# Performance work log

Measured on AMD Instinct MI355X. Metric: run time of the kernel, lower is better.

Reference implementation:

```python
import jax, jax.numpy as jnp
import numpy as np

D = 128      # d_model
H = 8        # n_heads
HD = D // H  # head_dim = 16
E = 256      # n_experts
R = 32       # kv_lora_rank
B, T = 4, 512
EPS = 1e-6


def _dense_init(k, fi, fo):
    s = float(1.0 / np.sqrt(fi))
    return jax.random.uniform(k, (fi, fo), minval=-s, maxval=s, dtype=jnp.float32)


def setup_inputs() -> dict:
    key = jax.random.key(0)
    ks = jax.random.split(key, 16)
    rng = np.random.RandomState(42)
    Q, _ = np.linalg.qr(rng.randn(D, D))
    glim = float(np.sqrt(6.0 / (D + D)))
    return {
        'x': jax.random.normal(ks[0], (B, T, D), dtype=jnp.float32),
        'g1': jnp.ones((D,), jnp.float32),
        'qW': _dense_init(ks[1], D, D), 'qb': jnp.zeros((D,), jnp.float32),
        'kdW': _dense_init(ks[2], D, R), 'kdb': jnp.zeros((R,), jnp.float32),
        'kuW': _dense_init(ks[3], R, 2 * D), 'kub': jnp.zeros((2 * D,), jnp.float32),
        'oW': _dense_init(ks[4], D, D), 'ob': jnp.zeros((D,), jnp.float32),
        'rot': jnp.asarray(Q, jnp.float32),
        'tq_scale': jnp.ones((D,), jnp.float32),
        's1W': _dense_init(ks[5], D, D), 's1b': jnp.zeros((D,), jnp.float32),
        's2W': _dense_init(ks[6], D, D), 's2b': jnp.zeros((D,), jnp.float32),
        'g2': jnp.ones((D,), jnp.float32),
        'gateW': _dense_init(ks[7], D, E), 'gateb': jnp.zeros((E,), jnp.float32),
        'expW': jax.random.uniform(ks[8], (E, D, D), minval=-glim, maxval=glim, dtype=jnp.float32),
        'm1W': _dense_init(ks[9], D, D), 'm1b': jnp.zeros((D,), jnp.float32),
        'm2W': _dense_init(ks[10], D, D), 'm2b': jnp.zeros((D,), jnp.float32),
    }


def _rmsnorm(x, g):
    return g * (x / jnp.sqrt(jnp.mean(x * x, axis=-1, keepdims=True) + EPS))


def _swiglu(x, w1, b1, w2, b2):
    gate = x @ w1 + b1
    return gate * jax.nn.sigmoid(gate) * (x @ w2 + b2)


def _mla(x, qW, qb, kdW, kdb, kuW, kub, oW, ob):
    b, t = x.shape[0], x.shape[1]
    q = (x @ qW + qb).reshape(b, t, H, HD)
    kv = ((x @ kdW + kdb) @ kuW + kub).reshape(b, t, H, 2 * HD)
    k, v = jnp.split(kv, 2, axis=-1)
    q = jax.nn.elu(q) + 1.0
    k = jax.nn.elu(k) + 1.0
    # linear attention: context[b,h,d,e] = sum_t k[b,t,h,d] v[b,t,h,e]
    context = jnp.einsum('bthd,bthe->bhde', k, v)
    out = jnp.einsum('bthd,bhde->bthe', q, context)
    k_sum = jnp.sum(k, axis=1)  # [b,h,d]
    z = 1.0 / (jnp.einsum('bthd,bhd->bth', q, k_sum) + EPS)
    out = out * z[..., None]
    return out.reshape(b, t, D) @ oW + ob


def _turbo_quant(x, rot, scale):
    x = x @ rot
    mag = jnp.sqrt(jnp.mean(x * x, axis=-1, keepdims=True) + EPS)
    phase = x / mag
    qp = jnp.clip(phase * 127.0, -127.0, 127.0) / 127.0
    phase = jax.lax.stop_gradient(qp - phase) + phase  # straight-through
    return phase * mag * scale


def _moe(h, gateW, gateb, expW, m1W, m1b, m2W, m2b):
    gate_scores = jax.nn.softmax(h @ gateW + gateb, axis=-1)  # [B,T,E]
    top_vals, top_idx = jax.lax.top_k(gate_scores, 2)
    top_w = top_vals / (jnp.sum(top_vals, axis=-1, keepdims=True) + EPS)
    # dense all-expert compute as in the original module
    eo = jnp.einsum('btd,edo->bteo', h, expW)  # [B,T,E,D]
    mask = jnp.sum(jax.nn.one_hot(top_idx, E, dtype=h.dtype) * top_w[..., None], axis=2)  # [B,T,E]
    wavg = jnp.einsum('bteo,bte->bto', eo, mask)
    wavg = _swiglu(wavg, m1W, m1b, m2W, m2b)
    diff_sq = jnp.square(eo - wavg[:, :, None, :])
    wvar = jnp.einsum('bteo,bte->bto', diff_sq, mask)
    consensus = jnp.exp(-jnp.mean(wvar, axis=-1))  # [B,T]
    return wavg, consensus


def reference(x, g1, qW, qb, kdW, kdb, kuW, kub, oW, ob, rot, tq_scale,
              s1W, s1b, s2W, s2b, g2, gateW, gateb, expW, m1W, m1b, m2W, m2b):
    attn_out = _turbo_quant(_mla(_rmsnorm(x, g1), qW, qb, kdW, kdb, kuW, kub, oW, ob), rot, tq_scale)
    x = x + _swiglu(attn_out, s1W, s1b, s2W, s2b)
    moe_out, consensus = _moe(_rmsnorm(x, g2), gateW, gateb, expW, m1W, m1b, m2W, m2b)
    return x + moe_out, consensus
```

## Files before the change

### kernel.cpp

```cpp
#include <hip/hip_runtime.h>
#include <math.h>

static constexpr int Dd    = 128;
static constexpr int NH    = 8;
static constexpr int NE    = 256;
static constexpr int RR    = 32;
static constexpr int TT    = 512;
static constexpr int NTOK  = 2048;
static constexpr int SLOTS = 256;
#define EPSF 1e-6f

static constexpr int FK_KV    = 0;
static constexpr int FD_CTX   = 32;
static constexpr int FD_OR    = 36;
static constexpr int FD_RG    = 37;
static constexpr int FD_ROOT  = 45;
static constexpr int FD_EXP   = 46;

__device__ __forceinline__ float elu1(float v) { return v > 0.f ? v + 1.f : expf(v); }
__device__ __forceinline__ float sigm(float v) { return 1.f / (1.f + expf(-v)); }

__device__ __forceinline__ void flag_add(int* p) {
  __hip_atomic_fetch_add(p, 1, __ATOMIC_RELEASE, __HIP_MEMORY_SCOPE_AGENT);
}
__device__ __forceinline__ void flag_wait(int* p, int tgt) {
  int c = 0;
  while (__hip_atomic_load(p, __ATOMIC_ACQUIRE, __HIP_MEMORY_SCOPE_AGENT) < tgt) {
    __builtin_amdgcn_s_sleep(2);
    if (++c > (1 << 27)) break;
  }
}

struct AParams {
  const float *x, *g1, *qW, *qb, *kdW, *kdb, *kuW, *kub, *oW, *ob, *rot, *tqs;
  const float *s1W, *s1b, *s2W, *s2b, *g2, *gateW, *gateb, *expW;
  const float *m1W, *m1b, *m2W, *m2b;
  float *kvbuf, *ctx, *ksum, *oR, *bR, *h2buf, *ybuf, *out;
  int *cnt, *slottok, *flags;
};

__global__ __launch_bounds__(512, 4) void k_all(AParams P) {
  const int tid = threadIdx.x;
  const int bid = blockIdx.x;
  const int t  = tid >> 7;
  const int j2 = tid & 127;
  const int lane = tid & 63;
  const int n0 = bid * 4;
  const int b = bid >> 7;

  __shared__ float sh[64 * 32];
  __shared__ float4 bufA[128];
  __shared__ float4 bufB[128];
  __shared__ float ws1[8], ws2[8];
  __shared__ float4 rtmp[2];
  __shared__ float wvS[4][4]; __shared__ int wiS[4][4];
  __shared__ float zS[4][4];
  __shared__ int sE[4][2]; __shared__ int sSlot[4][2]; __shared__ float sWt[4][2];
  __shared__ __align__(16) float hT[128 * 20];
  __shared__ float4 y1T[128], y2T[128], inT[128], sT[128];

  float4* kpart4 = (float4*)hT;
  float4* kdT4   = (float4*)(hT + 1024);

  const float xv_s = P.x[(n0 + t) * Dd + j2];
  {
    float v = xv_s * xv_s;
#pragma unroll
    for (int o = 32; o > 0; o >>= 1) v += __shfl_xor(v, o, 64);
    if (lane == 0) ws1[tid >> 6] = v;
  }
  __syncthreads();
  {
    float ss = ws1[2 * t] + ws1[2 * t + 1];
    ((float*)&bufB[j2])[t] = P.g1[j2] * xv_s * rsqrtf(ss * (1.f / 128.f) + EPSF);
  }
  __syncthreads();

  {
    float acc = 0.f;
    const float* Wp = P.qW + j2;
#pragma unroll 8
    for (int i = 0; i < 128; i++) acc += ((const float*)&bufB[i])[t] * Wp[i * Dd];
    ((float*)&bufA[j2])[t] = elu1(acc + P.qb[j2]);
  }

  if (tid < 256) {
    int col = tid & 31, ksp = tid >> 5;
    float a0 = 0, a1 = 0, a2 = 0, a3 = 0;
    const float* Wp = P.kdW + (ksp * 16) * RR + col;
#pragma unroll
    for (int i = 0; i < 16; i++) {
      float4 h4 = bufB[ksp * 16 + i];
      float w = Wp[i * RR];
      a0 += h4.x * w; a1 += h4.y * w; a2 += h4.z * w; a3 += h4.w * w;
    }
    kpart4[ksp * 32 + col] = make_float4(a0, a1, a2, a3);
  }
  __syncthreads();
  if (tid < 32) {
    float bb = P.kdb[tid];
    float s0 = bb, s1 = bb, s2 = bb, s3 = bb;
#pragma unroll
    for (int k = 0; k < 8; k++) {
      float4 p = kpart4[k * 32 + tid];
      s0 += p.x; s1 += p.y; s2 += p.z; s3 += p.w;
    }
    kdT4[tid] = make_float4(s0, s1, s2, s3);
  }
  __syncthreads();

  if (tid < 256) {
    const int col = tid;
    float a0 = 0, a1 = 0, a2 = 0, a3 = 0;
    const float* Wp = P.kuW + col;
#pragma unroll
    for (int r = 0; r < 32; r++) {
      float4 k4 = kdT4[r];
      float w = Wp[r * 256];
      a0 += k4.x * w; a1 += k4.y * w; a2 += k4.z * w; a3 += k4.w * w;
    }
    float bb = P.kub[col];
    bool isk = (col & 31) < 16;
    float v0 = a0 + bb, v1 = a1 + bb, v2 = a2 + bb, v3 = a3 + bb;
    P.kvbuf[(n0 + 0) * 256 + col] = isk ? elu1(v0) : v0;
    P.kvbuf[(n0 + 1) * 256 + col] = isk ? elu1(v1) : v1;
    P.kvbuf[(n0 + 2) * 256 + col] = isk ? elu1(v2) : v2;
    P.kvbuf[(n0 + 3) * 256 + col] = isk ? elu1(v3) : v3;
  }
  __threadfence();
  __syncthreads();
  if (tid == 0) flag_add(&P.flags[FK_KV + b * 8 + ((bid & 127) >> 4)]);

  if (bid < 256) {
    const int bh = bid >> 3, c = bid & 7;
    const int bb = bh >> 3, h = bh & 7;
    if (tid == 0) flag_wait(&P.flags[FK_KV + bb * 8 + c], 16);
    __syncthreads();
    __threadfence();
#pragma unroll
    for (int r = 0; r < 4; r++) {
      int lin = r * 512 + tid;
      int tok = lin >> 5, off = lin & 31;
      sh[lin] = P.kvbuf[((bb * TT + c * 64 + tok) * 256) + h * 32 + off];
    }
    __syncthreads();
    if (tid < 256) {
      const int d = tid >> 4, e = tid & 15;
      float acc = 0.f, ks = 0.f;
#pragma unroll 4
      for (int tk = 0; tk < 64; tk++) {
        float kk = sh[tk * 32 + d];
        acc += kk * sh[tk * 32 + 16 + e];
        ks += kk;
      }
      atomicAdd(&P.ctx[bh * 256 + d * 16 + e], acc);
      if (e == 0) atomicAdd(&P.ksum[bh * 16 + d], ks);
    }
    __threadfence();
    __syncthreads();
    if (tid == 0) flag_add(&P.flags[FD_CTX + bb]);
  } else if (bid < 288) {
    int idx = (bid - 256) * 512 + tid;
    int row = idx >> 7, col = idx & 127;
    const float* ow = P.oW + row * 128;
    float acc = 0.f;
#pragma unroll 8
    for (int k = 0; k < 128; k++) acc += ow[k] * P.rot[k * 128 + col];
    P.oR[idx] = acc;
    __threadfence();
    __syncthreads();
    if (tid == 0) flag_add(&P.flags[FD_OR]);
  } else if (bid == 288) {
    if (tid < 128) {
      float acc = 0.f;
#pragma unroll 8
      for (int k = 0; k < 128; k++) acc += P.ob[k] * P.rot[k * 128 + tid];
      P.bR[tid] = acc;
    }
    __threadfence();
    __syncthreads();
    if (tid == 0) flag_add(&P.flags[FD_OR]);
  }

  if (tid == 0) flag_wait(&P.flags[FD_CTX + b], 64);
  if (tid == 1) flag_wait(&P.flags[FD_OR], 33);
  __syncthreads();
  __threadfence();

  if (tid < 128) {
    int h = j2 >> 4, e = j2 & 15;
    const float* cpt = P.ctx + (b * NH + h) * 256;
    const float* kpt = P.ksum + (b * NH + h) * 16;
    float num[4] = {0, 0, 0, 0}, den[4] = {0, 0, 0, 0};
#pragma unroll
    for (int d = 0; d < 16; d++) {
      float cx = cpt[d * 16 + e], ks = kpt[d];
      float4 q4 = bufA[h * 16 + d];
      num[0] += q4.x * cx; num[1] += q4.y * cx; num[2] += q4.z * cx; num[3] += q4.w * cx;
      den[0] += q4.x * ks; den[1] += q4.y * ks; den[2] += q4.z * ks; den[3] += q4.w * ks;
    }
#pragma unroll
    for (int tt = 0; tt < 4; tt++) ((float*)&bufB[j2])[tt] = num[tt] / (den[tt] + EPSF);
  }
  __syncthreads();

  {
    float acc = 0.f;
    const float* Wp = P.oR + j2;
#pragma unroll 8
    for (int i = 0; i < 128; i++) acc += ((const float*)&bufB[i])[t] * Wp[i * Dd];
    float tot = acc + P.bR[j2];
    float v = tot * tot;
#pragma unroll
    for (int o = 32; o > 0; o >>= 1) v += __shfl_xor(v, o, 64);
    if (lane == 0) ws1[tid >> 6] = v;
    __syncthreads();
    float ss = ws1[2 * t] + ws1[2 * t + 1];
    float mag = sqrtf(ss * (1.f / 128.f) + EPSF);
    float zc = fminf(fmaxf(tot, -mag), mag);
    ((float*)&bufA[j2])[t] = zc * P.tqs[j2];
  }
  __syncthreads();

  float xn_s;
  {
    float a1 = 0.f, a2 = 0.f;
    const float* W1 = P.s1W + j2;
    const float* W2 = P.s2W + j2;
#pragma unroll 8
    for (int i = 0; i < 128; i++) {
      float h = ((const float*)&bufA[i])[t];
      a1 += h * W1[i * Dd];
      a2 += h * W2[i * Dd];
    }
    float gv = a1 + P.s1b[j2], uv = a2 + P.s2b[j2];
    xn_s = xv_s + gv * sigm(gv) * uv;
    float v = xn_s * xn_s;
#pragma unroll
    for (int o = 32; o > 0; o >>= 1) v += __shfl_xor(v, o, 64);
    if (lane == 0) ws2[tid >> 6] = v;
    ((float*)&bufB[j2])[t] = P.g2[j2] * xn_s;
  }
  __syncthreads();

  float val[4]; float r2v[4];
  {
#pragma unroll
    for (int tt = 0; tt < 4; tt++)
      r2v[tt] = rsqrtf((ws2[2 * tt] + ws2[2 * tt + 1]) * (1.f / 128.f) + EPSF);
    if (tid < 256) {
      const int col = tid;
      float a[4] = {0, 0, 0, 0};
      const float* Wp = P.gateW + col;
#pragma unroll 4
      for (int i = 0; i < 128; i++) {
        float4 h4 = bufB[i];
        float w = Wp[i * NE];
        a[0] += h4.x * w; a[1] += h4.y * w; a[2] += h4.z * w; a[3] += h4.w * w;
      }
      float bb = P.gateb[col];
#pragma unroll
      for (int tt = 0; tt < 4; tt++) val[tt] = a[tt] * r2v[tt] + bb;
    }
    P.h2buf[(n0 + t) * Dd + j2] = P.g2[j2] * xn_s * r2v[t];
  }
  __syncthreads();

  float m1[4]; int i1[4];
  {
    if (tid < 256) {
      float bv[4]; int bi[4];
#pragma unroll
      for (int tt = 0; tt < 4; tt++) { bv[tt] = val[tt]; bi[tt] = tid; }
#pragma unroll
      for (int o = 32; o > 0; o >>= 1) {
#pragma unroll
        for (int tt = 0; tt < 4; tt++) {
          float wv = __shfl_xor(bv[tt], o, 64);
          int wi = __shfl_xor(bi[tt], o, 64);
          if (wv > bv[tt] || (wv == bv[tt] && wi < bi[tt])) { bv[tt] = wv; bi[tt] = wi; }
        }
      }
      if (lane == 0) {
#pragma unroll
        for (int tt = 0; tt < 4; tt++) { wvS[tid >> 6][tt] = bv[tt]; wiS[tid >> 6][tt] = bi[tt]; }
      }
    }
    __syncthreads();
    if (tid < 256) {
#pragma unroll
      for (int tt = 0; tt < 4; tt++) {
        m1[tt] = wvS[0][tt]; i1[tt] = wiS[0][tt];
#pragma unroll
        for (int w = 1; w < 4; w++) {
          float cv = wvS[w][tt]; int ci = wiS[w][tt];
          if (cv > m1[tt] || (cv == m1[tt] && ci < i1[tt])) { m1[tt] = cv; i1[tt] = ci; }
        }
      }
    }
    __syncthreads();
  }
  float m2[4]; int i2[4];
  {
    if (tid < 256) {
      float bv[4]; int bi[4];
#pragma unroll
      for (int tt = 0; tt < 4; tt++) {
        bv[tt] = (tid == i1[tt]) ? -INFINITY : val[tt];
        bi[tt] = tid;
      }
#pragma unroll
      for (int o = 32; o > 0; o >>= 1) {
#pragma unroll
        for (int tt = 0; tt < 4; tt++) {
          float wv = __shfl_xor(bv[tt], o, 64);
          int wi = __shfl_xor(bi[tt], o, 64);
          if (wv > bv[tt] || (wv == bv[tt] && wi < bi[tt])) { bv[tt] = wv; bi[tt] = wi; }
        }
      }
      if (lane == 0) {
#pragma unroll
        for (int tt = 0; tt < 4; tt++) { wvS[tid >> 6][tt] = bv[tt]; wiS[tid >> 6][tt] = bi[tt]; }
      }
    }
    __syncthreads();
    if (tid < 256) {
#pragma unroll
      for (int tt = 0; tt < 4; tt++) {
        m2[tt] = wvS[0][tt]; i2[tt] = wiS[0][tt];
#pragma unroll
        for (int w = 1; w < 4; w++) {
          float cv = wvS[w][tt]; int ci = wiS[w][tt];
          if (cv > m2[tt] || (cv == m2[tt] && ci < i2[tt])) { m2[tt] = cv; i2[tt] = ci; }
        }
      }
    }
    __syncthreads();
  }
  {
    if (tid < 256) {
      float v[4];
#pragma unroll
      for (int tt = 0; tt < 4; tt++) v[tt] = expf(val[tt] - m1[tt]);
#pragma unroll
      for (int o = 32; o > 0; o >>= 1) {
#pragma unroll
        for (int tt = 0; tt < 4; tt++) v[tt] += __shfl_xor(v[tt], o, 64);
      }
      if (lane == 0) {
#pragma unroll
        for (int tt = 0; tt < 4; tt++) zS[tid >> 6][tt] = v[tt];
      }
    }
    __syncthreads();
  }
  if (tid < 4) {
    int tt = tid, tok = n0 + tt;
    float Z = zS[0][tt] + zS[1][tt] + zS[2][tt] + zS[3][tt];
    float p1 = 1.f / Z;
    float p2 = expf(m2[tt] - m1[tt]) / Z;
    float s = p1 + p2 + EPSF;
    int e1 = i1[tt], e2 = i2[tt];
    int s1 = atomicAdd(&P.cnt[e1], 1); if (s1 > SLOTS - 1) s1 = SLOTS - 1;
    int s2 = atomicAdd(&P.cnt[e2], 1); if (s2 > SLOTS - 1) s2 = SLOTS - 1;
    int sl1 = e1 * SLOTS + s1, sl2 = e2 * SLOTS + s2;
    P.slottok[sl1] = tok; P.slottok[sl2] = tok;
    sE[tt][0] = e1; sE[tt][1] = e2;
    sSlot[tt][0] = sl1; sSlot[tt][1] = sl2;
    sWt[tt][0] = p1 / s; sWt[tt][1] = p2 / s;
  }

  __threadfence();
  __syncthreads();
  if (tid == 0) {
    int grp = bid >> 6;
    int prev = __hip_atomic_fetch_add(&P.flags[FD_RG + grp], 1,
                                      __ATOMIC_ACQ_REL, __HIP_MEMORY_SCOPE_AGENT);
    if (prev == 63) flag_add(&P.flags[FD_ROOT]);
    flag_wait(&P.flags[FD_ROOT], 8);
  }
  __syncthreads();
  __threadfence();

  {
    const int e = bid >> 1, sub = bid & 1;
    int n = __hip_atomic_load(&P.cnt[e], __ATOMIC_RELAXED, __HIP_MEMORY_SCOPE_AGENT);
    if (n > SLOTS) n = SLOTS;
    const int base = e * SLOTS;
    const float* Wp = P.expW + (size_t)e * Dd * Dd + j2;
    for (int t0 = sub * 16; t0 < n; t0 += 32) {
      int m = n - t0; if (m > 16) m = 16;
      __syncthreads();
      for (int tt = t; tt < m; tt += 4) {
        int tok = P.slottok[base + t0 + tt];
        hT[j2 * 20 + tt] = P.h2buf[tok * Dd + j2];
      }
      __syncthreads();
      float acc[4] = {0, 0, 0, 0};
#pragma unroll 8
      for (int i = 0; i < 128; i++) {
        float w = Wp[i * Dd];
        float4 h4 = *(const float4*)&hT[i * 20 + t * 4];
        acc[0] += h4.x * w; acc[1] += h4.y * w; acc[2] += h4.z * w; acc[3] += h4.w * w;
      }
#pragma unroll
      for (int k = 0; k < 4; k++) {
        int tt = t * 4 + k;
        if (tt < m) P.ybuf[(size_t)(base + t0 + tt) * Dd + j2] = acc[k];
      }
    }
    __threadfence();
    __syncthreads();
    if (tid == 0) flag_add(&P.flags[FD_EXP + e]);
  }

  if (tid < 8) {
    int tt = tid >> 1, sl = tid & 1;
    flag_wait(&P.flags[FD_EXP + sE[tt][sl]], 2);
  }
  __syncthreads();
  __threadfence();

  {
    float y1 = P.ybuf[(size_t)sSlot[t][0] * Dd + j2];
    float y2 = P.ybuf[(size_t)sSlot[t][1] * Dd + j2];
    ((float*)&y1T[j2])[t] = y1;
    ((float*)&y2T[j2])[t] = y2;
    ((float*)&inT[j2])[t] = sWt[t][0] * y1 + sWt[t][1] * y2;
  }
  __syncthreads();

  {
    float a1 = 0.f, a2 = 0.f;
    const float* W1 = P.m1W + j2;
    const float* W2 = P.m2W + j2;
#pragma unroll 8
    for (int i = 0; i < 128; i++) {
      float h = ((const float*)&inT[i])[t];
      a1 += h * W1[i * Dd];
      a2 += h * W2[i * Dd];
    }
    float gv = a1 + P.m1b[j2], uv = a2 + P.m2b[j2];
    float sv = gv * sigm(gv) * uv;
    ((float*)&sT[j2])[t] = sv;
    P.out[(n0 + t) * Dd + j2] = xn_s + sv;
  }
  __syncthreads();

  if (tid < 128) {
    float v[4];
#pragma unroll
    for (int tt = 0; tt < 4; tt++) {
      float sv = ((const float*)&sT[j2])[tt];
      float d1 = ((const float*)&y1T[j2])[tt] - sv;
      float d2 = ((const float*)&y2T[j2])[tt] - sv;
      v[tt] = sWt[tt][0] * d1 * d1 + sWt[tt][1] * d2 * d2;
    }
#pragma unroll
    for (int o = 32; o > 0; o >>= 1) {
#pragma unroll
      for (int tt = 0; tt < 4; tt++) v[tt] += __shfl_xor(v[tt], o, 64);
    }
    if (lane == 0) rtmp[tid >> 6] = make_float4(v[0], v[1], v[2], v[3]);
  }
  __syncthreads();
  if (tid < 4) {
    float s = ((const float*)&rtmp[0])[tid] + ((const float*)&rtmp[1])[tid];
    P.out[NTOK * Dd + n0 + tid] = expf(-s * (1.f / 128.f));
  }
}

__global__ __launch_bounds__(512) void k_pre_fb(
    const float* __restrict__ x, const float* __restrict__ g1,
    const float* __restrict__ qW, const float* __restrict__ qb,
    const float* __restrict__ kdW, const float* __restrict__ kdb,
    const float* __restrict__ kuW, const float* __restrict__ kub,
    const float* __restrict__ oW, const float* __restrict__ ob,
    const float* __restrict__ rot,
    float* __restrict__ qbuf, float* __restrict__ kvbuf,
    float* __restrict__ ctx, float* __restrict__ ksum,
    int* __restrict__ cnt,
    float* __restrict__ oR, float* __restrict__ bR) {
  const int tid = threadIdx.x;
  const int bid = blockIdx.x;
  const int j = tid & 127, g = tid >> 7;
  const int lane = tid & 63;
  const int n0 = bid * 4;

  __shared__ float4 h1T[128];
  __shared__ float4 part[3][128];
  __shared__ float4 kpart[8][32];
  __shared__ float4 kdT[32];
  __shared__ float4 kupart[256];
  __shared__ float4 rtmp[2];

  if (bid == 0) {
    for (int i = tid; i < 32 * 256; i += 512) ctx[i] = 0.f;
    ksum[tid] = 0.f;
    if (tid < NE) cnt[tid] = 0;
  }

  float xv[4];
  if (tid < 128) {
    float v[4];
#pragma unroll
    for (int t = 0; t < 4; t++) { xv[t] = x[(n0 + t) * Dd + j]; v[t] = xv[t] * xv[t]; }
#pragma unroll
    for (int o = 32; o > 0; o >>= 1) {
#pragma unroll
      for (int t = 0; t < 4; t++) v[t] += __shfl_xor(v[t], o, 64);
    }
    if (lane == 0) rtmp[tid >> 6] = make_float4(v[0], v[1], v[2], v[3]);
  }
  __syncthreads();
  if (tid < 128) {
    float g1j = g1[j];
#pragma unroll
    for (int t = 0; t < 4; t++) {
      float ss = ((const float*)&rtmp[0])[t] + ((const float*)&rtmp[1])[t];
      ((float*)&h1T[j])[t] = g1j * xv[t] * rsqrtf(ss * (1.f / 128.f) + EPSF);
    }
  }
  __syncthreads();

  {
    float a0 = 0, a1 = 0, a2 = 0, a3 = 0;
    const float* Wp = qW + (g * 32) * Dd + j;
#pragma unroll 16
    for (int i = 0; i < 32; i++) {
      float4 h4 = h1T[g * 32 + i];
      float w = Wp[i * Dd];
      a0 += h4.x * w; a1 += h4.y * w; a2 += h4.z * w; a3 += h4.w * w;
    }
    if (g) part[g - 1][j] = make_float4(a0, a1, a2, a3);
    __syncthreads();
    if (g == 0) {
      float4 p0 = part[0][j], p1 = part[1][j], p2 = part[2][j];
      float bb = qb[j];
      qbuf[(n0 + 0) * Dd + j] = elu1(a0 + p0.x + p1.x + p2.x + bb);
      qbuf[(n0 + 1) * Dd + j] = elu1(a1 + p0.y + p1.y + p2.y + bb);
      qbuf[(n0 + 2) * Dd + j] = elu1(a2 + p0.z + p1.z + p2.z + bb);
      qbuf[(n0 + 3) * Dd + j] = elu1(a3 + p0.w + p1.w + p2.w + bb);
    }
    __syncthreads();
  }

  if (tid < 256) {
    int col = tid & 31, ksp = tid >> 5;
    float a0 = 0, a1 = 0, a2 = 0, a3 = 0;
    const float* Wp = kdW + (ksp * 16) * RR + col;
// ... 453 lines not shown
#pragma unroll
    for (int t = 0; t < 4; t++) {
      float sv = ((const float*)&sT[j])[t];
      float d1 = ((const float*)&y1T[j])[t] - sv;
      float d2 = ((const float*)&y2T[j])[t] - sv;
      v[t] = sWt[t][0] * d1 * d1 + sWt[t][1] * d2 * d2;
    }
#pragma unroll
    for (int o = 32; o > 0; o >>= 1) {
#pragma unroll
      for (int t = 0; t < 4; t++) v[t] += __shfl_xor(v[t], o, 64);
    }
    if (lane == 0) rtmp[tid >> 6] = make_float4(v[0], v[1], v[2], v[3]);
  }
  __syncthreads();
  if (tid < 4) {
    float s = ((const float*)&rtmp[0])[tid] + ((const float*)&rtmp[1])[tid];
    out[NTOK * Dd + n0 + tid] = expf(-s * (1.f / 128.f));
  }
}

extern "C" void kernel_launch(void* const* d_in, const int* in_sizes, int n_in,
                              void* d_out, int out_size, void* d_ws, size_t ws_size,
                              hipStream_t stream) {
  const float* x   = (const float*)d_in[0];
  const float* g1  = (const float*)d_in[1];
  const float* qW  = (const float*)d_in[2];
  const float* qb  = (const float*)d_in[3];
  const float* kdW = (const float*)d_in[4];
  const float* kdb = (const float*)d_in[5];
  const float* kuW = (const float*)d_in[6];
  const float* kub = (const float*)d_in[7];
  const float* oW  = (const float*)d_in[8];
  const float* ob  = (const float*)d_in[9];
  const float* rot = (const float*)d_in[10];
  const float* tqs = (const float*)d_in[11];
  const float* s1W = (const float*)d_in[12];
  const float* s1b = (const float*)d_in[13];
  const float* s2W = (const float*)d_in[14];
  const float* s2b = (const float*)d_in[15];
  const float* g2  = (const float*)d_in[16];
  const float* gW  = (const float*)d_in[17];
  const float* gb  = (const float*)d_in[18];
  const float* eW  = (const float*)d_in[19];
  const float* m1W = (const float*)d_in[20];
  const float* m1b = (const float*)d_in[21];
  const float* m2W = (const float*)d_in[22];
  const float* m2b = (const float*)d_in[23];
  float* out = (float*)d_out;
  float* ws  = (float*)d_ws;

  float* ctx     = ws;
  float* ksum    = ws + 8192;
  int*   cnt     = (int*)(ws + 8704);
  int*   flags   = (int*)(ws + 8960);
  float* oR      = ws + 9472;
  float* bR      = ws + 25856;
  float* kvbuf   = ws + 25984;
  float* h2buf   = ws + 550272;
  float* ybuf    = ws + 812416;
  int*   slottok = (int*)(ws + 9201024);
  float* qbuf    = ws + 9266560;
  float* xnbuf   = ws + 9528704;
  float* gw      = ws + 9790848;
  int*   tokslot = (int*)(ws + 9794944);

  hipMemsetAsync(ws, 0, (8192 + 512 + 256 + 512) * sizeof(float), stream);

  AParams p;
  p.x = x; p.g1 = g1; p.qW = qW; p.qb = qb; p.kdW = kdW; p.kdb = kdb;
  p.kuW = kuW; p.kub = kub; p.oW = oW; p.ob = ob; p.rot = rot; p.tqs = tqs;
  p.s1W = s1W; p.s1b = s1b; p.s2W = s2W; p.s2b = s2b; p.g2 = g2;
  p.gateW = gW; p.gateb = gb; p.expW = eW;
  p.m1W = m1W; p.m1b = m1b; p.m2W = m2W; p.m2b = m2b;
  p.kvbuf = kvbuf; p.ctx = ctx; p.ksum = ksum; p.oR = oR; p.bR = bR;
  p.h2buf = h2buf; p.ybuf = ybuf; p.out = out;
  p.cnt = cnt; p.slottok = slottok; p.flags = flags;

  void* args[] = {(void*)&p};
  hipError_t err = hipErrorUnknown;
  int nb = 0;
  if (hipOccupancyMaxActiveBlocksPerMultiprocessor(
          &nb, reinterpret_cast<const void*>(&k_all), 512, 0) == hipSuccess &&
      nb >= 2) {
    err = hipLaunchCooperativeKernel((void*)k_all, dim3(NTOK / 4), dim3(512),
                                     args, 0u, stream);
  }
  if (err == hipSuccess) return;

  k_pre_fb<<<NTOK / 4, 512, 0, stream>>>(x, g1, qW, qb, kdW, kdb, kuW, kub,
                                         oW, ob, rot, qbuf, kvbuf, ctx, ksum,
                                         cnt, oR, bR);
  k_ctx_fb<<<256, 256, 0, stream>>>(kvbuf, ctx, ksum);
  k_mid_fb<<<NTOK / 4, 512, 0, stream>>>(x, qbuf, ctx, ksum, oR, bR, tqs,
                                         s1W, s1b, s2W, s2b, g2, gW, gb,
                                         xnbuf, h2buf, gw, tokslot, slottok, cnt);
  k_exp_fb<<<NE * 2, 512, 0, stream>>>(h2buf, slottok, cnt, eW, ybuf);
  k_post_fb<<<NTOK / 4, 512, 0, stream>>>(xnbuf, ybuf, tokslot, gw,
                                          m1W, m1b, m2W, m2b, out);
}
```

Before: 164.5 us.

## Process sixteen tokens per block in fused cooperative kernel, shrinking grid to 128

The persistent cooperative kernel now handles 16 tokens per block instead of 4, so each weight load feeds four tokens per thread in every projection. The grid drops from 512 to 128 blocks, and the context and expert phases loop over several tasks per block. The two-level grid barrier becomes a single counter. Fewer blocks means less barrier and flag overhead and more weight reuse, at the cost of using only 128 of the GPU's compute units, more serial work per block, and higher register pressure.

```diff
diff --git a/kernel.cpp b/kernel.cpp
--- a/kernel.cpp
+++ b/kernel.cpp
@@ -8,12 +8,13 @@
 static constexpr int TT    = 512;
 static constexpr int NTOK  = 2048;
 static constexpr int SLOTS = 256;
+static constexpr int TPB   = 16;
+static constexpr int GRID  = NTOK / TPB;
 #define EPSF 1e-6f
 
 static constexpr int FK_KV    = 0;
 static constexpr int FD_CTX   = 32;
 static constexpr int FD_OR    = 36;
-static constexpr int FD_RG    = 37;
 static constexpr int FD_ROOT  = 45;
 static constexpr int FD_EXP   = 46;
 
@@ -39,147 +40,152 @@
   int *cnt, *slottok, *flags;
 };
 
-__global__ __launch_bounds__(512, 4) void k_all(AParams P) {
+__global__ __launch_bounds__(512) void k_all(AParams P) {
   const int tid = threadIdx.x;
   const int bid = blockIdx.x;
-  const int t  = tid >> 7;
+  const int tg = tid >> 7;
   const int j2 = tid & 127;
   const int lane = tid & 63;
-  const int n0 = bid * 4;
-  const int b = bid >> 7;
-
-  __shared__ float sh[64 * 32];
-  __shared__ float4 bufA[128];
-  __shared__ float4 bufB[128];
-  __shared__ float ws1[8], ws2[8];
-  __shared__ float4 rtmp[2];
+  const int wv = tid >> 6;
+  const int n0 = bid * TPB;
+  const int b = bid >> 5;
+
+  __shared__ float bufA[128][16];
+  __shared__ float bufB[128][16];
+  __shared__ float kdT[RR][16];
+  __shared__ float wsA[8][4], wsB[8][4];
+  __shared__ float r2S[16];
   __shared__ float wvS[4][4]; __shared__ int wiS[4][4];
   __shared__ float zS[4][4];
-  __shared__ int sE[4][2]; __shared__ int sSlot[4][2]; __shared__ float sWt[4][2];
-  __shared__ __align__(16) float hT[128 * 20];
-  __shared__ float4 y1T[128], y2T[128], inT[128], sT[128];
-
-  float4* kpart4 = (float4*)hT;
-  float4* kdT4   = (float4*)(hT + 1024);
-
-  const float xv_s = P.x[(n0 + t) * Dd + j2];
-  {
-    float v = xv_s * xv_s;
-#pragma unroll
-    for (int o = 32; o > 0; o >>= 1) v += __shfl_xor(v, o, 64);
-    if (lane == 0) ws1[tid >> 6] = v;
-  }
-  __syncthreads();
-  {
-    float ss = ws1[2 * t] + ws1[2 * t + 1];
-    ((float*)&bufB[j2])[t] = P.g1[j2] * xv_s * rsqrtf(ss * (1.f / 128.f) + EPSF);
-  }
-  __syncthreads();
-
-  {
+  __shared__ int sE[16][2]; __shared__ int sSlot[16][2]; __shared__ float sWt[16][2];
+  __shared__ __align__(16) float arena[2560];
+
+  float xv_r[4];
+  {
+    float v[4];
+#pragma unroll
+    for (int r = 0; r < 4; r++) {
+      xv_r[r] = P.x[(n0 + tg * 4 + r) * Dd + j2];
+      v[r] = xv_r[r] * xv_r[r];
+    }
+#pragma unroll
+    for (int o = 32; o > 0; o >>= 1)
+#pragma unroll
+      for (int r = 0; r < 4; r++) v[r] += __shfl_xor(v[r], o, 64);
+    if (lane == 0) {
+      wsA[wv][0] = v[0]; wsA[wv][1] = v[1]; wsA[wv][2] = v[2]; wsA[wv][3] = v[3];
+    }
+  }
+  __syncthreads();
+  {
+    float g1j = P.g1[j2];
+#pragma unroll
+    for (int r = 0; r < 4; r++) {
+      float ss = wsA[2 * tg][r] + wsA[2 * tg + 1][r];
+      bufB[j2][tg * 4 + r] = g1j * xv_r[r] * rsqrtf(ss * (1.f / 128.f) + EPSF);
+    }
+  }
+  __syncthreads();
+
+  {
+    float acc[4] = {0, 0, 0, 0};
+    const float* Wp = P.qW + j2;
+#pragma unroll 4
+    for (int i = 0; i < 128; i++) {
+      float w = Wp[i * Dd];
+#pragma unroll
+      for (int r = 0; r < 4; r++) acc[r] += bufB[i][tg * 4 + r] * w;
+    }
+    float bb = P.qb[j2];
+#pragma unroll
+    for (int r = 0; r < 4; r++) bufA[j2][tg * 4 + r] = elu1(acc[r] + bb);
+  }
+
+  {
+    int col = tid & 31, tok = tid >> 5;
     float acc = 0.f;
-    const float* Wp = P.qW + j2;
-#pragma unroll 8
-    for (int i = 0; i < 128; i++) acc += ((const float*)&bufB[i])[t] * Wp[i * Dd];
-    ((float*)&bufA[j2])[t] = elu1(acc + P.qb[j2]);
-  }
-
-  if (tid < 256) {
-    int col = tid & 31, ksp = tid >> 5;
-    float a0 = 0, a1 = 0, a2 = 0, a3 = 0;
-    const float* Wp = P.kdW + (ksp * 16) * RR + col;
-#pragma unroll
-    for (int i = 0; i < 16; i++) {
-      float4 h4 = bufB[ksp * 16 + i];
-      float w = Wp[i * RR];
-      a0 += h4.x * w; a1 += h4.y * w; a2 += h4.z * w; a3 += h4.w * w;
-    }
-    kpart4[ksp * 32 + col] = make_float4(a0, a1, a2, a3);
-  }
-  __syncthreads();
-  if (tid < 32) {
-    float bb = P.kdb[tid];
-    float s0 = bb, s1 = bb, s2 = bb, s3 = bb;
-#pragma unroll
-    for (int k = 0; k < 8; k++) {
-      float4 p = kpart4[k * 32 + tid];
-      s0 += p.x; s1 += p.y; s2 += p.z; s3 += p.w;
-    }
-    kdT4[tid] = make_float4(s0, s1, s2, s3);
-  }
-  __syncthreads();
-
-  if (tid < 256) {
-    const int col = tid;
-    float a0 = 0, a1 = 0, a2 = 0, a3 = 0;
+    const float* Wp = P.kdW + col;
+#pragma unroll 4
+    for (int i = 0; i < 128; i++) acc += bufB[i][tok] * Wp[i * RR];
+    kdT[col][tok] = acc + P.kdb[col];
+  }
+  __syncthreads();
+
+  {
+    int col = tid & 255, half = tid >> 8;
+    float acc[8] = {0, 0, 0, 0, 0, 0, 0, 0};
     const float* Wp = P.kuW + col;
 #pragma unroll
     for (int r = 0; r < 32; r++) {
-      float4 k4 = kdT4[r];
       float w = Wp[r * 256];
-      a0 += k4.x * w; a1 += k4.y * w; a2 += k4.z * w; a3 += k4.w * w;
+#pragma unroll
+      for (int m = 0; m < 8; m++) acc[m] += kdT[r][half * 8 + m] * w;
     }
     float bb = P.kub[col];
     bool isk = (col & 31) < 16;
-    float v0 = a0 + bb, v1 = a1 + bb, v2 = a2 + bb, v3 = a3 + bb;
-    P.kvbuf[(n0 + 0) * 256 + col] = isk ? elu1(v0) : v0;
-    P.kvbuf[(n0 + 1) * 256 + col] = isk ? elu1(v1) : v1;
-    P.kvbuf[(n0 + 2) * 256 + col] = isk ? elu1(v2) : v2;
-    P.kvbuf[(n0 + 3) * 256 + col] = isk ? elu1(v3) : v3;
+#pragma unroll
+    for (int m = 0; m < 8; m++) {
+      float v = acc[m] + bb;
+      P.kvbuf[(n0 + half * 8 + m) * 256 + col] = isk ? elu1(v) : v;
+    }
   }
   __threadfence();
   __syncthreads();
-  if (tid == 0) flag_add(&P.flags[FK_KV + b * 8 + ((bid & 127) >> 4)]);
-
-  if (bid < 256) {
-    const int bh = bid >> 3, c = bid & 7;
-    const int bb = bh >> 3, h = bh & 7;
-    if (tid == 0) flag_wait(&P.flags[FK_KV + bb * 8 + c], 16);
-    __syncthreads();
-    __threadfence();
-#pragma unroll
-    for (int r = 0; r < 4; r++) {
-      int lin = r * 512 + tid;
-      int tok = lin >> 5, off = lin & 31;
-      sh[lin] = P.kvbuf[((bb * TT + c * 64 + tok) * 256) + h * 32 + off];
-    }
-    __syncthreads();
-    if (tid < 256) {
-      const int d = tid >> 4, e = tid & 15;
-      float acc = 0.f, ks = 0.f;
-#pragma unroll 4
-      for (int tk = 0; tk < 64; tk++) {
-        float kk = sh[tk * 32 + d];
-        acc += kk * sh[tk * 32 + 16 + e];
-        ks += kk;
-      }
-      atomicAdd(&P.ctx[bh * 256 + d * 16 + e], acc);
-      if (e == 0) atomicAdd(&P.ksum[bh * 16 + d], ks);
-    }
-    __threadfence();
-    __syncthreads();
-    if (tid == 0) flag_add(&P.flags[FD_CTX + bb]);
-  } else if (bid < 288) {
-    int idx = (bid - 256) * 512 + tid;
+  if (tid == 0) flag_add(&P.flags[FK_KV + b * 8 + ((bid >> 2) & 7)]);
+
+  if (bid < 32) {
+    int idx = bid * 512 + tid;
     int row = idx >> 7, col = idx & 127;
     const float* ow = P.oW + row * 128;
     float acc = 0.f;
 #pragma unroll 8
     for (int k = 0; k < 128; k++) acc += ow[k] * P.rot[k * 128 + col];
     P.oR[idx] = acc;
-    __threadfence();
-    __syncthreads();
+    __threadfence(); __syncthreads();
     if (tid == 0) flag_add(&P.flags[FD_OR]);
-  } else if (bid == 288) {
+  } else if (bid == 32) {
     if (tid < 128) {
       float acc = 0.f;
 #pragma unroll 8
       for (int k = 0; k < 128; k++) acc += P.ob[k] * P.rot[k * 128 + tid];
       P.bR[tid] = acc;
     }
-    __threadfence();
-    __syncthreads();
+    __threadfence(); __syncthreads();
     if (tid == 0) flag_add(&P.flags[FD_OR]);
+  }
+
+  {
+    float* sh = arena;
+    for (int k = 0; k < 2; k++) {
+      int task = bid + k * 128;
+      int bh = task >> 3, c = task & 7;
+      int bb2 = bh >> 3, h = bh & 7;
+      if (tid == 0) flag_wait(&P.flags[FK_KV + bb2 * 8 + c], 4);
+      __syncthreads();
+      __threadfence();
+#pragma unroll
+      for (int r = 0; r < 4; r++) {
+        int lin = r * 512 + tid;
+        int tok = lin >> 5, off = lin & 31;
+        sh[lin] = P.kvbuf[((bb2 * TT + c * 64 + tok) * 256) + h * 32 + off];
+      }
+      __syncthreads();
+      if (tid < 256) {
+        int d = tid >> 4, e = tid & 15;
+        float acc = 0.f, ks = 0.f;
+#pragma unroll 4
+        for (int tk = 0; tk < 64; tk++) {
+          float kk = sh[tk * 32 + d];
+          acc += kk * sh[tk * 32 + 16 + e];
+          ks += kk;
+        }
+        atomicAdd(&P.ctx[bh * 256 + d * 16 + e], acc);
+        if (e == 0) atomicAdd(&P.ksum[bh * 16 + d], ks);
+      }
+      __threadfence();
+      __syncthreads();
+      if (tid == 0) flag_add(&P.flags[FD_CTX + bb2]);
+    }
   }
 
   if (tid == 0) flag_wait(&P.flags[FD_CTX + b], 64);
@@ -187,7 +193,7 @@
   __syncthreads();
   __threadfence();
 
-  if (tid < 128) {
+  {
     int h = j2 >> 4, e = j2 & 15;
     const float* cpt = P.ctx + (b * NH + h) * 256;
     const float* kpt = P.ksum + (b * NH + h) * 16;
@@ -195,277 +201,332 @@
 #pragma unroll
     for (int d = 0; d < 16; d++) {
       float cx = cpt[d * 16 + e], ks = kpt[d];
-      float4 q4 = bufA[h * 16 + d];
-      num[0] += q4.x * cx; num[1] += q4.y * cx; num[2] += q4.z * cx; num[3] += q4.w * cx;
-      den[0] += q4.x * ks; den[1] += q4.y * ks; den[2] += q4.z * ks; den[3] += q4.w * ks;
-    }
-#pragma unroll
-    for (int tt = 0; tt < 4; tt++) ((float*)&bufB[j2])[tt] = num[tt] / (den[tt] + EPSF);
-  }
-  __syncthreads();
-
-  {
-    float acc = 0.f;
+#pragma unroll
+      for (int r = 0; r < 4; r++) {
+        float qv = bufA[h * 16 + d][tg * 4 + r];
+        num[r] += qv * cx; den[r] += qv * ks;
+      }
+    }
+#pragma unroll
+    for (int r = 0; r < 4; r++) bufB[j2][tg * 4 + r] = num[r] / (den[r] + EPSF);
+  }
+  __syncthreads();
+
+  {
+    float acc[4] = {0, 0, 0, 0};
     const float* Wp = P.oR + j2;
-#pragma unroll 8
-    for (int i = 0; i < 128; i++) acc += ((const float*)&bufB[i])[t] * Wp[i * Dd];
-    float tot = acc + P.bR[j2];
-    float v = tot * tot;
-#pragma unroll
-    for (int o = 32; o > 0; o >>= 1) v += __shfl_xor(v, o, 64);
-    if (lane == 0) ws1[tid >> 6] = v;
-    __syncthreads();
-    float ss = ws1[2 * t] + ws1[2 * t + 1];
-    float mag = sqrtf(ss * (1.f / 128.f) + EPSF);
-    float zc = fminf(fmaxf(tot, -mag), mag);
-    ((float*)&bufA[j2])[t] = zc * P.tqs[j2];
-  }
-  __syncthreads();
-
-  float xn_s;
-  {
-    float a1 = 0.f, a2 = 0.f;
+#pragma unroll 4
+    for (int i = 0; i < 128; i++) {
+      float w = Wp[i * Dd];
+#pragma unroll
+      for (int r = 0; r < 4; r++) acc[r] += bufB[i][tg * 4 + r] * w;
+    }
+    float bRj = P.bR[j2];
+    float tot[4], v[4];
+#pragma unroll
+    for (int r = 0; r < 4; r++) { tot[r] = acc[r] + bRj; v[r] = tot[r] * tot[r]; }
+#pragma unroll
+    for (int o = 32; o > 0; o >>= 1)
+#pragma unroll
+      for (int r = 0; r < 4; r++) v[r] += __shfl_xor(v[r], o, 64);
+    if (lane == 0) {
+      wsA[wv][0] = v[0]; wsA[wv][1] = v[1]; wsA[wv][2] = v[2]; wsA[wv][3] = v[3];
+    }
+    __syncthreads();
+    float scj = P.tqs[j2];
+#pragma unroll
+    for (int r = 0; r < 4; r++) {
+      float ss = wsA[2 * tg][r] + wsA[2 * tg + 1][r];
+      float mag = sqrtf(ss * (1.f / 128.f) + EPSF);
+      float zc = fminf(fmaxf(tot[r], -mag), mag);
+      bufA[j2][tg * 4 + r] = zc * scj;
+    }
+  }
+  __syncthreads();
+
+  float xn_r[4];
+  {
+    float a1[4] = {0, 0, 0, 0}, a2[4] = {0, 0, 0, 0};
     const float* W1 = P.s1W + j2;
     const float* W2 = P.s2W + j2;
+#pragma unroll 4
+    for (int i = 0; i < 128; i++) {
+      float w1 = W1[i * Dd], w2 = W2[i * Dd];
+#pragma unroll
+      for (int r = 0; r < 4; r++) {
+        float h = bufA[i][tg * 4 + r];
+        a1[r] += h * w1; a2[r] += h * w2;
+      }
+    }
+    float b1 = P.s1b[j2], b2 = P.s2b[j2], g2j = P.g2[j2];
+    float v[4];
+#pragma unroll
+    for (int r = 0; r < 4; r++) {
+      float gv = a1[r] + b1, uv = a2[r] + b2;
+      xn_r[r] = xv_r[r] + gv * sigm(gv) * uv;
+      v[r] = xn_r[r] * xn_r[r];
+      bufB[j2][tg * 4 + r] = g2j * xn_r[r];
+    }
+#pragma unroll
+    for (int o = 32; o > 0; o >>= 1)
+#pragma unroll
+      for (int r = 0; r < 4; r++) v[r] += __shfl_xor(v[r], o, 64);
+    if (lane == 0) {
+      wsB[wv][0] = v[0]; wsB[wv][1] = v[1]; wsB[wv][2] = v[2]; wsB[wv][3] = v[3];
+    }
+  }
+  __syncthreads();
+  if (tid < 16) {
+    int tgo = tid >> 2, r = tid & 3;
+    r2S[tid] = rsqrtf((wsB[2 * tgo][r] + wsB[2 * tgo + 1][r]) * (1.f / 128.f) + EPSF);
+  }
+  __syncthreads();
+  {
+#pragma unroll
+    for (int r = 0; r < 4; r++)
+      P.h2buf[(n0 + tg * 4 + r) * Dd + j2] = bufB[j2][tg * 4 + r] * r2S[tg * 4 + r];
+  }
+
+  {
+    float4* gpart = (float4*)arena;
+    for (int grp = 0; grp < 4; grp++) {
+      float val[4]; float r2v[4];
+#pragma unroll
+      for (int t = 0; t < 4; t++) r2v[t] = r2S[grp * 4 + t];
+      {
+        int col = tid & 255, kh = tid >> 8;
+        float a0 = 0, a1 = 0, a2 = 0, a3 = 0;
+        const float* Wp = P.gateW + (kh * 64) * NE + col;
 #pragma unroll 8
-    for (int i = 0; i < 128; i++) {
-      float h = ((const float*)&bufA[i])[t];
-      a1 += h * W1[i * Dd];
-      a2 += h * W2[i * Dd];
-    }
-    float gv = a1 + P.s1b[j2], uv = a2 + P.s2b[j2];
-    xn_s = xv_s + gv * sigm(gv) * uv;
-    float v = xn_s * xn_s;
-#pragma unroll
-    for (int o = 32; o > 0; o >>= 1) v += __shfl_xor(v, o, 64);
-    if (lane == 0) ws2[tid >> 6] = v;
-    ((float*)&bufB[j2])[t] = P.g2[j2] * xn_s;
-  }
-  __syncthreads();
-
-  float val[4]; float r2v[4];
-  {
-#pragma unroll
-    for (int tt = 0; tt < 4; tt++)
-      r2v[tt] = rsqrtf((ws2[2 * tt] + ws2[2 * tt + 1]) * (1.f / 128.f) + EPSF);
-    if (tid < 256) {
-      const int col = tid;
-      float a[4] = {0, 0, 0, 0};
-      const float* Wp = P.gateW + col;
-#pragma unroll 4
-      for (int i = 0; i < 128; i++) {
-        float4 h4 = bufB[i];
-        float w = Wp[i * NE];
-        a[0] += h4.x * w; a[1] += h4.y * w; a[2] += h4.z * w; a[3] += h4.w * w;
-      }
-      float bb = P.gateb[col];
-#pragma unroll
-      for (int tt = 0; tt < 4; tt++) val[tt] = a[tt] * r2v[tt] + bb;
-    }
-    P.h2buf[(n0 + t) * Dd + j2] = P.g2[j2] * xn_s * r2v[t];
-  }
-  __syncthreads();
-
-  float m1[4]; int i1[4];
-  {
-    if (tid < 256) {
-      float bv[4]; int bi[4];
-#pragma unroll
-      for (int tt = 0; tt < 4; tt++) { bv[tt] = val[tt]; bi[tt] = tid; }
-#pragma unroll
-      for (int o = 32; o > 0; o >>= 1) {
-#pragma unroll
-        for (int tt = 0; tt < 4; tt++) {
-          float wv = __shfl_xor(bv[tt], o, 64);
-          int wi = __shfl_xor(bi[tt], o, 64);
-          if (wv > bv[tt] || (wv == bv[tt] && wi < bi[tt])) { bv[tt] = wv; bi[tt] = wi; }
-        }
-      }
-      if (lane == 0) {
-#pragma unroll
-        for (int tt = 0; tt < 4; tt++) { wvS[tid >> 6][tt] = bv[tt]; wiS[tid >> 6][tt] = bi[tt]; }
-      }
-    }
-    __syncthreads();
-    if (tid < 256) {
-#pragma unroll
-      for (int tt = 0; tt < 4; tt++) {
-        m1[tt] = wvS[0][tt]; i1[tt] = wiS[0][tt];
-#pragma unroll
-        for (int w = 1; w < 4; w++) {
-          float cv = wvS[w][tt]; int ci = wiS[w][tt];
-          if (cv > m1[tt] || (cv == m1[tt] && ci < i1[tt])) { m1[tt] = cv; i1[tt] = ci; }
-        }
-      }
-    }
-    __syncthreads();
-  }
-  float m2[4]; int i2[4];
-  {
-    if (tid < 256) {
-      float bv[4]; int bi[4];
-#pragma unroll
-      for (int tt = 0; tt < 4; tt++) {
-        bv[tt] = (tid == i1[tt]) ? -INFINITY : val[tt];
-        bi[tt] = tid;
-      }
-#pragma unroll
-      for (int o = 32; o > 0; o >>= 1) {
-#pragma unroll
-        for (int tt = 0; tt < 4; tt++) {
-          float wv = __shfl_xor(bv[tt], o, 64);
-          int wi = __shfl_xor(bi[tt], o, 64);
-          if (wv > bv[tt] || (wv == bv[tt] && wi < bi[tt])) { bv[tt] = wv; bi[tt] = wi; }
-        }
-      }
-      if (lane == 0) {
-#pragma unroll
-        for (int tt = 0; tt < 4; tt++) { wvS[tid >> 6][tt] = bv[tt]; wiS[tid >> 6][tt] = bi[tt]; }
-      }
-    }
-    __syncthreads();
-    if (tid < 256) {
-#pragma unroll
-      for (int tt = 0; tt < 4; tt++) {
-        m2[tt] = wvS[0][tt]; i2[tt] = wiS[0][tt];
-#pragma unroll
-        for (int w = 1; w < 4; w++) {
-          float cv = wvS[w][tt]; int ci = wiS[w][tt];
-          if (cv > m2[tt] || (cv == m2[tt] && ci < i2[tt])) { m2[tt] = cv; i2[tt] = ci; }
-        }
-      }
-    }
-    __syncthreads();
-  }
-  {
-    if (tid < 256) {
-      float v[4];
-#pragma unroll
-      for (int tt = 0; tt < 4; tt++) v[tt] = expf(val[tt] - m1[tt]);
-#pragma unroll
-      for (int o = 32; o > 0; o >>= 1) {
-#pragma unroll
-        for (int tt = 0; tt < 4; tt++) v[tt] += __shfl_xor(v[tt], o, 64);
-      }
-      if (lane == 0) {
-#pragma unroll
-        for (int tt = 0; tt < 4; tt++) zS[tid >> 6][tt] = v[tt];
-      }
-    }
-    __syncthreads();
-  }
-  if (tid < 4) {
-    int tt = tid, tok = n0 + tt;
-    float Z = zS[0][tt] + zS[1][tt] + zS[2][tt] + zS[3][tt];
-    float p1 = 1.f / Z;
-    float p2 = expf(m2[tt] - m1[tt]) / Z;
-    float s = p1 + p2 + EPSF;
-    int e1 = i1[tt], e2 = i2[tt];
-    int s1 = atomicAdd(&P.cnt[e1], 1); if (s1 > SLOTS - 1) s1 = SLOTS - 1;
-    int s2 = atomicAdd(&P.cnt[e2], 1); if (s2 > SLOTS - 1) s2 = SLOTS - 1;
-    int sl1 = e1 * SLOTS + s1, sl2 = e2 * SLOTS + s2;
-    P.slottok[sl1] = tok; P.slottok[sl2] = tok;
-    sE[tt][0] = e1; sE[tt][1] = e2;
-    sSlot[tt][0] = sl1; sSlot[tt][1] = sl2;
-    sWt[tt][0] = p1 / s; sWt[tt][1] = p2 / s;
+        for (int i = 0; i < 64; i++) {
+          float4 h4 = *(const float4*)&bufB[kh * 64 + i][grp * 4];
+          float w = Wp[i * NE];
+          a0 += h4.x * w; a1 += h4.y * w; a2 += h4.z * w; a3 += h4.w * w;
+        }
+        if (kh) gpart[col] = make_float4(a0, a1, a2, a3);
+        __syncthreads();
+        if (!kh) {
+          float4 p = gpart[col];
+          float bb = P.gateb[col];
+          val[0] = (a0 + p.x) * r2v[0] + bb; val[1] = (a1 + p.y) * r2v[1] + bb;
+          val[2] = (a2 + p.z) * r2v[2] + bb; val[3] = (a3 + p.w) * r2v[3] + bb;
+        }
+      }
+      __syncthreads();
+
+      float m1[4]; int i1[4];
+      {
+        if (tid < 256) {
+          float bv[4]; int bi[4];
+#pragma unroll
+          for (int t = 0; t < 4; t++) { bv[t] = val[t]; bi[t] = tid; }
+#pragma unroll
+          for (int o = 32; o > 0; o >>= 1) {
+#pragma unroll
+            for (int t = 0; t < 4; t++) {
+              float wvv = __shfl_xor(bv[t], o, 64);
+              int wii = __shfl_xor(bi[t], o, 64);
+              if (wvv > bv[t] || (wvv == bv[t] && wii < bi[t])) { bv[t] = wvv; bi[t] = wii; }
+            }
+          }
+          if (lane == 0) {
+#pragma unroll
+            for (int t = 0; t < 4; t++) { wvS[tid >> 6][t] = bv[t]; wiS[tid >> 6][t] = bi[t]; }
+          }
+        }
+        __syncthreads();
+        if (tid < 256) {
+#pragma unroll
+          for (int t = 0; t < 4; t++) {
+            m1[t] = wvS[0][t]; i1[t] = wiS[0][t];
+#pragma unroll
+            for (int w = 1; w < 4; w++) {
+              float cv = wvS[w][t]; int ci = wiS[w][t];
+              if (cv > m1[t] || (cv == m1[t] && ci < i1[t])) { m1[t] = cv; i1[t] = ci; }
+            }
+          }
+        }
+        __syncthreads();
+      }
+      float m2[4]; int i2[4];
+      {
+        if (tid < 256) {
+          float bv[4]; int bi[4];
+#pragma unroll
+          for (int t = 0; t < 4; t++) {
+            bv[t] = (tid == i1[t]) ? -INFINITY : val[t];
+            bi[t] = tid;
+          }
+#pragma unroll
+          for (int o = 32; o > 0; o >>= 1) {
+#pragma unroll
+            for (int t = 0; t < 4; t++) {
+              float wvv = __shfl_xor(bv[t], o, 64);
+              int wii = __shfl_xor(bi[t], o, 64);
+              if (wvv > bv[t] || (wvv == bv[t] && wii < bi[t])) { bv[t] = wvv; bi[t] = wii; }
+            }
+          }
+          if (lane == 0) {
+#pragma unroll
+            for (int t = 0; t < 4; t++) { wvS[tid >> 6][t] = bv[t]; wiS[tid >> 6][t] = bi[t]; }
+          }
+        }
+        __syncthreads();
+        if (tid < 256) {
+#pragma unroll
+          for (int t = 0; t < 4; t++) {
+            m2[t] = wvS[0][t]; i2[t] = wiS[0][t];
+#pragma unroll
+            for (int w = 1; w < 4; w++) {
+              float cv = wvS[w][t]; int ci = wiS[w][t];
+              if (cv > m2[t] || (cv == m2[t] && ci < i2[t])) { m2[t] = cv; i2[t] = ci; }
+            }
+          }
+        }
+        __syncthreads();
+      }
+      {
+        if (tid < 256) {
+          float v[4];
+#pragma unroll
+          for (int t = 0; t < 4; t++) v[t] = expf(val[t] - m1[t]);
+#pragma unroll
+          for (int o = 32; o > 0; o >>= 1) {
+#pragma unroll
+            for (int t = 0; t < 4; t++) v[t] += __shfl_xor(v[t], o, 64);
+          }
+          if (lane == 0) {
+#pragma unroll
+            for (int t = 0; t < 4; t++) zS[tid >> 6][t] = v[t];
+          }
+        }
+        __syncthreads();
+      }
+      if (tid < 4) {
+        int t = tid, tok = n0 + grp * 4 + t;
+        float Z = zS[0][t] + zS[1][t] + zS[2][t] + zS[3][t];
+        float p1 = 1.f / Z;
+        float p2 = expf(m2[t] - m1[t]) / Z;
+        float s = p1 + p2 + EPSF;
+        int e1 = i1[t], e2 = i2[t];
+        int s1 = atomicAdd(&P.cnt[e1], 1); if (s1 > SLOTS - 1) s1 = SLOTS - 1;
+        int s2 = atomicAdd(&P.cnt[e2], 1); if (s2 > SLOTS - 1) s2 = SLOTS - 1;
+        int sl1 = e1 * SLOTS + s1, sl2 = e2 * SLOTS + s2;
+        P.slottok[sl1] = tok; P.slottok[sl2] = tok;
+        sE[grp * 4 + t][0] = e1; sE[grp * 4 + t][1] = e2;
+        sSlot[grp * 4 + t][0] = sl1; sSlot[grp * 4 + t][1] = sl2;
+        sWt[grp * 4 + t][0] = p1 / s; sWt[grp * 4 + t][1] = p2 / s;
+      }
+      __syncthreads();
+    }
   }
 
   __threadfence();
   __syncthreads();
   if (tid == 0) {
-    int grp = bid >> 6;
-    int prev = __hip_atomic_fetch_add(&P.flags[FD_RG + grp], 1,
-                                      __ATOMIC_ACQ_REL, __HIP_MEMORY_SCOPE_AGENT);
-    if (prev == 63) flag_add(&P.flags[FD_ROOT]);
-    flag_wait(&P.flags[FD_ROOT], 8);
+    flag_add(&P.flags[FD_ROOT]);
+    flag_wait(&P.flags[FD_ROOT], 128);
   }
   __syncthreads();
   __threadfence();
 
   {
-    const int e = bid >> 1, sub = bid & 1;
-    int n = __hip_atomic_load(&P.cnt[e], __ATOMIC_RELAXED, __HIP_MEMORY_SCOPE_AGENT);
-    if (n > SLOTS) n = SLOTS;
-    const int base = e * SLOTS;
-    const float* Wp = P.expW + (size_t)e * Dd * Dd + j2;
-    for (int t0 = sub * 16; t0 < n; t0 += 32) {
-      int m = n - t0; if (m > 16) m = 16;
+    float* hT = arena;
+    for (int k = 0; k < 4; k++) {
+      int task = bid + k * 128;
+      int e = task >> 1, sub = task & 1;
+      int n = __hip_atomic_load(&P.cnt[e], __ATOMIC_RELAXED, __HIP_MEMORY_SCOPE_AGENT);
+      if (n > SLOTS) n = SLOTS;
+      const int base = e * SLOTS;
+      const float* Wp = P.expW + (size_t)e * Dd * Dd + j2;
+      for (int t0 = sub * 16; t0 < n; t0 += 32) {
+        int m = n - t0; if (m > 16) m = 16;
+        __syncthreads();
+        for (int tt = tg; tt < m; tt += 4) {
+          int tok = P.slottok[base + t0 + tt];
+          hT[j2 * 20 + tt] = P.h2buf[tok * Dd + j2];
+        }
+        __syncthreads();
+        float acc[4] = {0, 0, 0, 0};
+#pragma unroll 8
+        for (int i = 0; i < 128; i++) {
+          float w = Wp[i * Dd];
+          float4 h4 = *(const float4*)&hT[i * 20 + tg * 4];
+          acc[0] += h4.x * w; acc[1] += h4.y * w; acc[2] += h4.z * w; acc[3] += h4.w * w;
+        }
+#pragma unroll
+        for (int q = 0; q < 4; q++) {
+          int tt = tg * 4 + q;
+          if (tt < m) P.ybuf[(size_t)(base + t0 + tt) * Dd + j2] = acc[q];
+        }
+      }
+      __threadfence();
       __syncthreads();
-      for (int tt = t; tt < m; tt += 4) {
-        int tok = P.slottok[base + t0 + tt];
-        hT[j2 * 20 + tt] = P.h2buf[tok * Dd + j2];
-      }
-      __syncthreads();
-      float acc[4] = {0, 0, 0, 0};
-#pragma unroll 8
-      for (int i = 0; i < 128; i++) {
-        float w = Wp[i * Dd];
-        float4 h4 = *(const float4*)&hT[i * 20 + t * 4];
-        acc[0] += h4.x * w; acc[1] += h4.y * w; acc[2] += h4.z * w; acc[3] += h4.w * w;
-      }
-#pragma unroll
-      for (int k = 0; k < 4; k++) {
-        int tt = t * 4 + k;
-        if (tt < m) P.ybuf[(size_t)(base + t0 + tt) * Dd + j2] = acc[k];
-      }
-    }
-    __threadfence();
-    __syncthreads();
-    if (tid == 0) flag_add(&P.flags[FD_EXP + e]);
-  }
-
-  if (tid < 8) {
-    int tt = tid >> 1, sl = tid & 1;
-    flag_wait(&P.flags[FD_EXP + sE[tt][sl]], 2);
+      if (tid == 0) flag_add(&P.flags[FD_EXP + e]);
+    }
+  }
+
+  if (tid < 32) {
+    int tok = tid >> 1, sl = tid & 1;
+    flag_wait(&P.flags[FD_EXP + sE[tok][sl]], 2);
   }
   __syncthreads();
   __threadfence();
 
-  {
-    float y1 = P.ybuf[(size_t)sSlot[t][0] * Dd + j2];
-    float y2 = P.ybuf[(size_t)sSlot[t][1] * Dd + j2];
-    ((float*)&y1T[j2])[t] = y1;
-    ((float*)&y2T[j2])[t] = y2;
-    ((float*)&inT[j2])[t] = sWt[t][0] * y1 + sWt[t][1] * y2;
-  }
-  __syncthreads();
-
-  {
-    float a1 = 0.f, a2 = 0.f;
+  float (*inT)[16] = (float(*)[16])arena;
+  float y1_r[4], y2_r[4];
+  {
+#pragma unroll
+    for (int r = 0; r < 4; r++) {
+      int tok = tg * 4 + r;
+      y1_r[r] = P.ybuf[(size_t)sSlot[tok][0] * Dd + j2];
+      y2_r[r] = P.ybuf[(size_t)sSlot[tok][1] * Dd + j2];
+      inT[j2][tok] = sWt[tok][0] * y1_r[r] + sWt[tok][1] * y2_r[r];
+    }
+  }
+  __syncthreads();
+  float sv_r[4];
+  {
+    float a1[4] = {0, 0, 0, 0}, a2[4] = {0, 0, 0, 0};
     const float* W1 = P.m1W + j2;
     const float* W2 = P.m2W + j2;
-#pragma unroll 8
+#pragma unroll 4
     for (int i = 0; i < 128; i++) {
-      float h = ((const float*)&inT[i])[t];
-      a1 += h * W1[i * Dd];
-      a2 += h * W2[i * Dd];
-    }
-    float gv = a1 + P.m1b[j2], uv = a2 + P.m2b[j2];
-    float sv = gv * sigm(gv) * uv;
-    ((float*)&sT[j2])[t] = sv;
-    P.out[(n0 + t) * Dd + j2] = xn_s + sv;
-  }
-  __syncthreads();
-
-  if (tid < 128) {
+      float w1 = W1[i * Dd], w2 = W2[i * Dd];
+#pragma unroll
+      for (int r = 0; r < 4; r++) {
+        float h = inT[i][tg * 4 + r];
+        a1[r] += h * w1; a2[r] += h * w2;
+      }
+    }
+    float b1 = P.m1b[j2], b2 = P.m2b[j2];
+#pragma unroll
+    for (int r = 0; r < 4; r++) {
+      float gv = a1[r] + b1, uv = a2[r] + b2;
+      sv_r[r] = gv * sigm(gv) * uv;
+      P.out[(n0 + tg * 4 + r) * Dd + j2] = xn_r[r] + sv_r[r];
+    }
+  }
+  {
     float v[4];
 #pragma unroll
-    for (int tt = 0; tt < 4; tt++) {
-      float sv = ((const float*)&sT[j2])[tt];
-      float d1 = ((const float*)&y1T[j2])[tt] - sv;
-      float d2 = ((const float*)&y2T[j2])[tt] - sv;
-      v[tt] = sWt[tt][0] * d1 * d1 + sWt[tt][1] * d2 * d2;
-    }
-#pragma unroll
-    for (int o = 32; o > 0; o >>= 1) {
-#pragma unroll
-      for (int tt = 0; tt < 4; tt++) v[tt] += __shfl_xor(v[tt], o, 64);
-    }
-    if (lane == 0) rtmp[tid >> 6] = make_float4(v[0], v[1], v[2], v[3]);
-  }
-  __syncthreads();
-  if (tid < 4) {
-    float s = ((const float*)&rtmp[0])[tid] + ((const float*)&rtmp[1])[tid];
+    for (int r = 0; r < 4; r++) {
+      int tok = tg * 4 + r;
+      float d1 = y1_r[r] - sv_r[r], d2 = y2_r[r] - sv_r[r];
+      v[r] = sWt[tok][0] * d1 * d1 + sWt[tok][1] * d2 * d2;
+    }
+#pragma unroll
+    for (int o = 32; o > 0; o >>= 1)
+#pragma unroll
+      for (int r = 0; r < 4; r++) v[r] += __shfl_xor(v[r], o, 64);
+    if (lane == 0) {
+      wsA[wv][0] = v[0]; wsA[wv][1] = v[1]; wsA[wv][2] = v[2]; wsA[wv][3] = v[3];
+    }
+  }
+  __syncthreads();
+  if (tid < 16) {
+    int tgo = tid >> 2, r = tid & 3;
+    float s = wsA[2 * tgo][r] + wsA[2 * tgo + 1][r];
     P.out[NTOK * Dd + n0 + tid] = expf(-s * (1.f / 128.f));
   }
 }
@@ -1085,8 +1146,8 @@
   int nb = 0;
   if (hipOccupancyMaxActiveBlocksPerMultiprocessor(
           &nb, reinterpret_cast<const void*>(&k_all), 512, 0) == hipSuccess &&
-      nb >= 2) {
-    err = hipLaunchCooperativeKernel((void*)k_all, dim3(NTOK / 4), dim3(512),
+      nb >= 1) {
+    err = hipLaunchCooperativeKernel((void*)k_all, dim3(GRID), dim3(512),
                                      args, 0u, stream);
   }
   if (err == hipSuccess) return;
```

New measurement: 163.3 us. No clear change (-0.8%).
